# Kernel optimization log

Measured on AMD Instinct MI355X. Metric: run time of the kernel, lower is better.

## Reference

```python
import jax, jax.numpy as jnp
import numpy as np

N_NODES = 100000
N_EDGES = 1250000
IN_CH = 128
OUT_CH = 64


def setup_inputs() -> dict:
    key = jax.random.key(0)
    k1, k2, k3, k4 = jax.random.split(key, 4)
    x = jax.random.normal(k1, (N_NODES, IN_CH), dtype=jnp.float32)
    edge_index = jax.random.randint(k2, (2, N_EDGES), 0, N_NODES, dtype=jnp.int64)
    edge_weight = jax.random.uniform(k3, (N_EDGES,), dtype=jnp.float32)
    # Xavier-uniform weight, zero bias (as in reset_parameters)
    limit = float(np.sqrt(6.0 / (IN_CH + OUT_CH)))
    W = jax.random.uniform(k4, (IN_CH, OUT_CH), dtype=jnp.float32, minval=-limit, maxval=limit)
    b = jnp.zeros((OUT_CH,), dtype=jnp.float32)
    return {"x": x, "edge_index": edge_index, "edge_weight": edge_weight, "W": W, "b": b}


def reference(x, edge_index, edge_weight, W, b):
    # Dense transform: [N, in] @ [in, out] -> [N, out]
    h = jnp.matmul(x, W)
    row, col = edge_index[0], edge_index[1]
    n = h.shape[0]
    # Weighted in-degree via scatter-add on destination (row)
    deg = jnp.zeros((n,), dtype=h.dtype).at[row].add(edge_weight)
    # deg^-0.5 with inf (deg==0) replaced by 0
    deg_inv_sqrt = jnp.where(deg == 0, jnp.zeros_like(deg), deg ** -0.5)
    norm = deg_inv_sqrt[row] * deg_inv_sqrt[col]  # [E]
    # Gather source features, normalize, scatter-add to destinations
    out = jnp.zeros_like(h).at[row].add(h[col] * norm[:, None])
    return out + b
```

## Files before the change

kernel.cpp:

```cpp
#include <hip/hip_runtime.h>

#define N_NODES 100000
#define N_EDGES 1250000
#define IN_CH 128
#define OUT_CH 64

#define NPB 128
#define ACCS2 33
#define NBINS 782
#define HPAD 784
#define BINCAP_DEF 2048
#define NB1 256
#define B1T 512
#define CH1 ((N_EDGES + NB1 - 1) / NB1)
#define MAXU ((CH1 + B1T - 1) / B1T)
#define GEMM_BLOCKS ((N_NODES + 127) / 128)

#define QSCALE 8192.0f
#define QBIAS_F 8388608.0f
#define QBIAS_U 8388608u
#define INV_QSCALE 1.220703125e-4f
#define SCALE_DEG 33554432.0f
#define INV_SCALE_DEG 2.9802322387695312e-08f

typedef __attribute__((ext_vector_type(8))) short short8;
typedef __attribute__((ext_vector_type(4))) float f32x4;

__device__ inline unsigned int f2bf(float f) {
    unsigned int u = __float_as_uint(f);
    unsigned int r = ((u >> 16) & 1u) + 0x7FFFu;
    return (u + r) >> 16;
}
__device__ inline float bf_lo(unsigned int p) { return __uint_as_float(p << 16); }
__device__ inline float bf_hi(unsigned int p) { return __uint_as_float(p & 0xFFFF0000u); }

__device__ inline unsigned long long qpacks(unsigned int p, float sc) {
    unsigned int lo = (unsigned int)__float2int_rn(fmaf(bf_lo(p), sc, QBIAS_F));
    unsigned int hi = (unsigned int)__float2int_rn(fmaf(bf_hi(p), sc, QBIAS_F));
    return ((unsigned long long)hi << 32) | (unsigned long long)lo;
}

__global__ __launch_bounds__(256) void init_kernel(const float* __restrict__ W,
                                                   unsigned int* __restrict__ Wb) {
    int g = blockIdx.x * 256 + threadIdx.x;
    int c = g >> 8;
    int t4 = (g >> 6) & 3;
    int l = g & 63;
    int q = l >> 4, r15 = l & 15;
    unsigned int o[4];
#pragma unroll
    for (int jj = 0; jj < 4; ++jj) {
        float f0 = W[(c * 32 + q * 8 + 2 * jj)     * OUT_CH + t4 * 16 + r15];
        float f1 = W[(c * 32 + q * 8 + 2 * jj + 1) * OUT_CH + t4 * 16 + r15];
        o[jj] = f2bf(f0) | (f2bf(f1) << 16);
    }
    *(uint4*)(Wb + (size_t)g * 4) = make_uint4(o[0], o[1], o[2], o[3]);
}

__global__ __launch_bounds__(512) void fused_kernel(const float* __restrict__ x,
                                                    const unsigned int* __restrict__ Wb,
                                                    const int* __restrict__ ei,
                                                    int* __restrict__ hist2d,
                                                    unsigned int* __restrict__ hs) {
    __shared__ int hist[NBINS];
    const int tid = threadIdx.x;

    if (blockIdx.x < NB1) {
        for (int i = tid; i < NBINS; i += B1T) hist[i] = 0;
        __syncthreads();

        const int e0 = blockIdx.x * CH1;
        const int e1 = (e0 + CH1 < N_EDGES) ? e0 + CH1 : N_EDGES;
#pragma unroll
        for (int u = 0; u < MAXU; ++u) {
            int e = e0 + tid + u * B1T;
            if (e < e1) atomicAdd(&hist[ei[e] >> 7], 1);
        }
        __syncthreads();

        int* hrow = hist2d + blockIdx.x * HPAD;
        for (int i = tid; i < NBINS; i += B1T) hrow[i] = hist[i];
    } else {
        const int blk  = blockIdx.x - NB1;
        const int w    = tid >> 6;
        const int lane = tid & 63;
        const int q    = lane >> 4, r15 = lane & 15;
        const int node = blk * 128 + w * 16 + r15;
        const int nl   = (node < N_NODES) ? node : N_NODES - 1;
        const float* xrow = x + (size_t)nl * IN_CH;

        f32x4 acc[4];
#pragma unroll
        for (int t = 0; t < 4; ++t) acc[t] = (f32x4){0.f, 0.f, 0.f, 0.f};

#pragma unroll
        for (int c = 0; c < 4; ++c) {
            float4 xa = *(const float4*)(xrow + c * 32 + q * 8);
            float4 xb = *(const float4*)(xrow + c * 32 + q * 8 + 4);
            short8 bfrag;
            bfrag[0] = (short)f2bf(xa.x); bfrag[1] = (short)f2bf(xa.y);
            bfrag[2] = (short)f2bf(xa.z); bfrag[3] = (short)f2bf(xa.w);
            bfrag[4] = (short)f2bf(xb.x); bfrag[5] = (short)f2bf(xb.y);
            bfrag[6] = (short)f2bf(xb.z); bfrag[7] = (short)f2bf(xb.w);
#pragma unroll
            for (int t = 0; t < 4; ++t) {
                short8 afrag = *(const short8*)(Wb + (size_t)((c * 4 + t) * 64 + lane) * 4);
                acc[t] = __builtin_amdgcn_mfma_f32_16x16x32_bf16(afrag, bfrag, acc[t], 0, 0, 0);
            }
        }

        if (node < N_NODES) {
#pragma unroll
            for (int t = 0; t < 4; ++t) {
                unsigned int p0 = f2bf(acc[t][0]) | (f2bf(acc[t][1]) << 16);
                unsigned int p1 = f2bf(acc[t][2]) | (f2bf(acc[t][3]) << 16);
                *(uint2*)(hs + (size_t)node * 32 + t * 8 + q * 2) = make_uint2(p0, p1);
            }
        }
    }
}

__global__ __launch_bounds__(256) void scan_kernel(const int* __restrict__ hist2d,
                                                   int* __restrict__ offs2d,
                                                   int* __restrict__ mtot,
                                                   int bincap) {
    __shared__ int tmp[256];
    const int b = blockIdx.x, t = threadIdx.x;
    int v = hist2d[t * HPAD + b];
    int acc = v;
    tmp[t] = acc;
    __syncthreads();
#pragma unroll
    for (int d = 1; d < 256; d <<= 1) {
        int add = (t >= d) ? tmp[t - d] : 0;
        __syncthreads();
        acc += add;
        tmp[t] = acc;
        __syncthreads();
    }
    offs2d[b * 256 + t] = b * bincap + (acc - v);
    if (t == 255) mtot[b] = acc;
}

__global__ __launch_bounds__(B1T) void scatter_kernel(const int* __restrict__ ei,
                                                      const float* __restrict__ ew,
                                                      const int* __restrict__ offs2d,
                                                      int2* __restrict__ brec,
                                                      int bincap) {
    __shared__ int rank[NBINS];
    __shared__ int base[NBINS];
    const int t = threadIdx.x;
    for (int i = t; i < NBINS; i += B1T) {
        rank[i] = 0;
        base[i] = offs2d[i * 256 + blockIdx.x];
    }
    __syncthreads();

    const int e0 = blockIdx.x * CH1;
    const int e1 = (e0 + CH1 < N_EDGES) ? e0 + CH1 : N_EDGES;
#pragma unroll
    for (int u = 0; u < MAXU; ++u) {
        int e = e0 + t + u * B1T;
        if (e < e1) {
            int row = ei[e];
            int col = ei[N_EDGES + e];
            float w = ew[e];
            int bb = row >> 7;
            int rk = atomicAdd(&rank[bb], 1);
            int idx = base[bb] + rk;
            if (idx < (bb + 1) * bincap)
                brec[idx] = make_int2(((row & 127) << 17) | col, __float_as_int(w));
        }
    }
}

__global__ __launch_bounds__(256) void bin2_kernel(const int* __restrict__ mtot,
                                                   const int2* __restrict__ brec,
                                                   float* __restrict__ dis_g,
                                                   int bincap) {
    __shared__ int deg[NPB];
    const int t = threadIdx.x;
    const int b = blockIdx.x;
    if (t < NPB) deg[t] = 0;
    __syncthreads();

    const int rbase = b * bincap;
    int m = mtot[b];
    if (m > bincap) m = bincap;

    for (int j = t; j < m; j += 256) {
        int2 rec = brec[rbase + j];
        atomicAdd(&deg[rec.x >> 17], __float2int_rn(__int_as_float(rec.y) * SCALE_DEG));
    }
    __syncthreads();

    int node = b * NPB + t;
    if (t < NPB && node < N_NODES) {
        float d = (float)deg[t] * INV_SCALE_DEG;
        dis_g[node] = (d == 0.0f) ? 0.0f : (1.0f / sqrtf(d));
    }
}

__global__ __launch_bounds__(512) void gather_kernel(const int* __restrict__ mtot,
                                                     const int2* __restrict__ brec,
                                                     const uint4* __restrict__ hs,
                                                     const float* __restrict__ dis,
                                                     const float* __restrict__ b,
                                                     float* __restrict__ out,
                                                     int bincap) {
    __shared__ unsigned long long acc[NPB * ACCS2];
    __shared__ int cnt[NPB];
    const int tid = threadIdx.x;
    const int blk = blockIdx.x;
    for (int k = tid; k < NPB * ACCS2; k += 512) acc[k] = 0ull;
    if (tid < NPB) cnt[tid] = 0;
    __syncthreads();

    const int rbase = blk * bincap;
    int m = mtot[blk];
    if (m > bincap) m = bincap;

    const int wid = tid >> 6, lane = tid & 63;
    const int sub = lane >> 3, l8 = lane & 7;

    for (int j0 = wid * 32; j0 < m; j0 += 256) {
        bool ok[4];
        int rec[4];
        uint4 p[4];
        float sc[4];
#pragma unroll
        for (int s = 0; s < 4; ++s) {
            int jj = j0 + 8 * s + sub;
            ok[s] = jj < m;
            rec[s] = ok[s] ? brec[rbase + jj].x : 0;
        }
#pragma unroll
        for (int s = 0; s < 4; ++s) {
            p[s] = ok[s] ? hs[(size_t)(rec[s] & 0x1FFFF) * 8 + l8]
                         : make_uint4(0, 0, 0, 0);
            sc[s] = ok[s] ? QSCALE * dis[rec[s] & 0x1FFFF] : 0.0f;
        }
#pragma unroll
        for (int s = 0; s < 4; ++s) {
            if (ok[s]) {
                int ba = (rec[s] >> 17) * ACCS2 + 4 * l8;
                atomicAdd(&acc[ba + 0], qpacks(p[s].x, sc[s]));
                atomicAdd(&acc[ba + 1], qpacks(p[s].y, sc[s]));
                atomicAdd(&acc[ba + 2], qpacks(p[s].z, sc[s]));
                atomicAdd(&acc[ba + 3], qpacks(p[s].w, sc[s]));
                if (l8 == 0) atomicAdd(&cnt[rec[s] >> 17], 1);
            }
        }
    }
    __syncthreads();

    const unsigned int* acc32 = (const unsigned int*)acc;
    float bc = b[lane];
    int half = lane & 1, slot = lane >> 1;
#pragma unroll 4
    for (int r = 0; r < 16; ++r) {
        int nl = wid * 16 + r;
        int node = blk * NPB + nl;
        if (node < N_NODES) {
            unsigned int raw = acc32[(nl * ACCS2 + slot) * 2 + half];
            int qsum = (int)(raw - (unsigned int)cnt[nl] * QBIAS_U);
            float di = dis[node] * INV_QSCALE;
            out[(size_t)node * OUT_CH + lane] = (float)qsum * di + bc;
        }
    }
}

extern "C" void kernel_launch(void* const* d_in, const int* in_sizes, int n_in,
                              void* d_out, int out_size, void* d_ws, size_t ws_size,
                              hipStream_t stream) {
    const float* x  = (const float*)d_in[0];
    const int*   ei = (const int*)d_in[1];
    const float* ew = (const float*)d_in[2];
    const float* W  = (const float*)d_in[3];
    const float* b  = (const float*)d_in[4];
    float* out = (float*)d_out;

    unsigned int* hs = (unsigned int*)d_ws;
    unsigned int* Wb = hs + (size_t)N_NODES * 32;
    int* hist2d = (int*)(Wb + 4096);
    int* offs2d = hist2d + NB1 * HPAD;
    int* mtot   = offs2d + NBINS * 256;
    float* dis  = (float*)(mtot + 800);
    int2* brec  = (int2*)(dis + N_NODES);
    size_t used = (size_t)N_NODES * 32 + 4096 + (size_t)NB1 * HPAD
                + (size_t)NBINS * 256 + 800 + (size_t)N_NODES;
    size_t rem  = (ws_size / 4 > used) ? ws_size / 4 - used : 0;
    int bincap  = (int)(rem / (2 * (size_t)NBINS));
    if (bincap > BINCAP_DEF) bincap = BINCAP_DEF;

    init_kernel<<<4, 256, 0, stream>>>(W, Wb);
    fused_kernel<<<NB1 + GEMM_BLOCKS, 512, 0, stream>>>(x, Wb, ei, hist2d, hs);
    scan_kernel<<<NBINS, 256, 0, stream>>>(hist2d, offs2d, mtot, bincap);
    scatter_kernel<<<NB1, B1T, 0, stream>>>(ei, ew, offs2d, brec, bincap);
    bin2_kernel<<<NBINS, 256, 0, stream>>>(mtot, brec, dis, bincap);
    gather_kernel<<<NBINS, 512, 0, stream>>>(mtot, brec, (const uint4*)hs,
                                             dis, b, out, bincap);
}
```

Measured before the change: 171.9 us.

## Sort edges locally per block in shared memory, drop scan and scatter kernels

The edge-binning block of the fused kernel now builds its histogram, scans it in shared memory and writes its edge records already grouped by destination bin, along with a per-block scan table. Bin-degree and gather kernels then read each bin's records from 256 per-chunk segments using that table, instead of from a globally scattered bin array. This removes the global scan and scatter kernels, two launches, and the random global scatter writes. In exchange the fused kernel reserves about 40 KB of static shared memory, which the GEMM blocks also pay for and which may lower their occupancy. The gather kernel also gains a 256-wide shared scan and a serial per-thread segment copy.

Result: slower. 178.0 us (+3.6%).

```diff
diff --git a/kernel.cpp b/kernel.cpp
--- a/kernel.cpp
+++ b/kernel.cpp
@@ -8,8 +8,8 @@
 #define NPB 128
 #define ACCS2 33
 #define NBINS 782
-#define HPAD 784
-#define BINCAP_DEF 2048
+#define LSTRIDE 783
+#define RECCAP 2048
 #define NB1 256
 #define B1T 512
 #define CH1 ((N_EDGES + NB1 - 1) / NB1)
@@ -60,26 +60,81 @@
 __global__ __launch_bounds__(512) void fused_kernel(const float* __restrict__ x,
                                                     const unsigned int* __restrict__ Wb,
                                                     const int* __restrict__ ei,
-                                                    int* __restrict__ hist2d,
+                                                    const float* __restrict__ ew,
+                                                    int* __restrict__ lscan2d,
+                                                    int2* __restrict__ brec,
                                                     unsigned int* __restrict__ hs) {
-    __shared__ int hist[NBINS];
+    __shared__ int2 srec[CH1];
+    __shared__ int shist[NBINS];
+    __shared__ int sscan[NBINS + 2];
+    __shared__ int ssum[256];
     const int tid = threadIdx.x;
 
     if (blockIdx.x < NB1) {
-        for (int i = tid; i < NBINS; i += B1T) hist[i] = 0;
+        for (int i = tid; i < NBINS; i += B1T) shist[i] = 0;
         __syncthreads();
 
         const int e0 = blockIdx.x * CH1;
-        const int e1 = (e0 + CH1 < N_EDGES) ? e0 + CH1 : N_EDGES;
+        const int total = (e0 + CH1 < N_EDGES) ? CH1 : N_EDGES - e0;
+
+        int rowv[MAXU], colv[MAXU];
+        float wv[MAXU];
 #pragma unroll
         for (int u = 0; u < MAXU; ++u) {
             int e = e0 + tid + u * B1T;
-            if (e < e1) atomicAdd(&hist[ei[e] >> 7], 1);
-        }
-        __syncthreads();
-
-        int* hrow = hist2d + blockIdx.x * HPAD;
-        for (int i = tid; i < NBINS; i += B1T) hrow[i] = hist[i];
+            bool ok = (tid + u * B1T) < total;
+            rowv[u] = ok ? ei[e] : -1;
+            colv[u] = ok ? ei[N_EDGES + e] : 0;
+            wv[u]   = ok ? ew[e] : 0.0f;
+            if (ok) atomicAdd(&shist[rowv[u] >> 7], 1);
+        }
+        __syncthreads();
+
+        int a0 = 0, a1 = 0, a2 = 0, a3 = 0, part = 0;
+        const int b0 = tid * 4;
+        if (tid < 256) {
+            a0 = (b0 + 0 < NBINS) ? shist[b0 + 0] : 0;
+            a1 = (b0 + 1 < NBINS) ? shist[b0 + 1] : 0;
+            a2 = (b0 + 2 < NBINS) ? shist[b0 + 2] : 0;
+            a3 = (b0 + 3 < NBINS) ? shist[b0 + 3] : 0;
+            part = a0 + a1 + a2 + a3;
+            ssum[tid] = part;
+        }
+        __syncthreads();
+#pragma unroll
+        for (int d = 1; d < 256; d <<= 1) {
+            int add = 0;
+            if (tid >= d && tid < 256) add = ssum[tid - d];
+            __syncthreads();
+            if (tid < 256) ssum[tid] += add;
+            __syncthreads();
+        }
+        if (tid < 256) {
+            int base = ssum[tid] - part;
+            if (b0 + 0 <= NBINS) sscan[b0 + 0] = base;
+            if (b0 + 1 <= NBINS) sscan[b0 + 1] = base + a0;
+            if (b0 + 2 <= NBINS) sscan[b0 + 2] = base + a0 + a1;
+            if (b0 + 3 <= NBINS) sscan[b0 + 3] = base + a0 + a1 + a2;
+        }
+        __syncthreads();
+
+        for (int i = tid; i < NBINS; i += B1T) shist[i] = 0;
+        __syncthreads();
+
+#pragma unroll
+        for (int u = 0; u < MAXU; ++u) {
+            if (rowv[u] >= 0) {
+                int bb = rowv[u] >> 7;
+                int rk = atomicAdd(&shist[bb], 1);
+                srec[sscan[bb] + rk] = make_int2(((rowv[u] & 127) << 17) | colv[u],
+                                                 __float_as_int(wv[u]));
+            }
+        }
+        __syncthreads();
+
+        for (int i = tid; i < total; i += B1T) brec[e0 + i] = srec[i];
+        int* lrow = lscan2d + blockIdx.x * LSTRIDE;
+        for (int i = tid; i <= NBINS; i += B1T) lrow[i] = sscan[i];
     } else {
         const int blk  = blockIdx.x - NB1;
         const int w    = tid >> 6;
@@ -120,76 +175,20 @@
     }
 }
 
-__global__ __launch_bounds__(256) void scan_kernel(const int* __restrict__ hist2d,
-                                                   int* __restrict__ offs2d,
-                                                   int* __restrict__ mtot,
-                                                   int bincap) {
-    __shared__ int tmp[256];
-    const int b = blockIdx.x, t = threadIdx.x;
-    int v = hist2d[t * HPAD + b];
-    int acc = v;
-    tmp[t] = acc;
-    __syncthreads();
-#pragma unroll
-    for (int d = 1; d < 256; d <<= 1) {
-        int add = (t >= d) ? tmp[t - d] : 0;
-        __syncthreads();
-        acc += add;
-        tmp[t] = acc;
-        __syncthreads();
-    }
-    offs2d[b * 256 + t] = b * bincap + (acc - v);
-    if (t == 255) mtot[b] = acc;
-}
-
-__global__ __launch_bounds__(B1T) void scatter_kernel(const int* __restrict__ ei,
-                                                      const float* __restrict__ ew,
-                                                      const int* __restrict__ offs2d,
-                                                      int2* __restrict__ brec,
-                                                      int bincap) {
-    __shared__ int rank[NBINS];
-    __shared__ int base[NBINS];
-    const int t = threadIdx.x;
-    for (int i = t; i < NBINS; i += B1T) {
-        rank[i] = 0;
-        base[i] = offs2d[i * 256 + blockIdx.x];
-    }
-    __syncthreads();
-
-    const int e0 = blockIdx.x * CH1;
-    const int e1 = (e0 + CH1 < N_EDGES) ? e0 + CH1 : N_EDGES;
-#pragma unroll
-    for (int u = 0; u < MAXU; ++u) {
-        int e = e0 + t + u * B1T;
-        if (e < e1) {
-            int row = ei[e];
-            int col = ei[N_EDGES + e];
-            float w = ew[e];
-            int bb = row >> 7;
-            int rk = atomicAdd(&rank[bb], 1);
-            int idx = base[bb] + rk;
-            if (idx < (bb + 1) * bincap)
-                brec[idx] = make_int2(((row & 127) << 17) | col, __float_as_int(w));
-        }
-    }
-}
-
-__global__ __launch_bounds__(256) void bin2_kernel(const int* __restrict__ mtot,
+__global__ __launch_bounds__(256) void bin2_kernel(const int* __restrict__ lscan2d,
                                                    const int2* __restrict__ brec,
-                                                   float* __restrict__ dis_g,
-                                                   int bincap) {
+                                                   float* __restrict__ dis_g) {
     __shared__ int deg[NPB];
     const int t = threadIdx.x;
     const int b = blockIdx.x;
     if (t < NPB) deg[t] = 0;
     __syncthreads();
 
-    const int rbase = b * bincap;
-    int m = mtot[b];
-    if (m > bincap) m = bincap;
-
-    for (int j = t; j < m; j += 256) {
-        int2 rec = brec[rbase + j];
+    int st = lscan2d[t * LSTRIDE + b];
+    int en = lscan2d[t * LSTRIDE + b + 1];
+    const int2* seg = brec + (size_t)t * CH1;
+    for (int j = st; j < en; ++j) {
+        int2 rec = seg[j];
         atomicAdd(&deg[rec.x >> 17], __float2int_rn(__int_as_float(rec.y) * SCALE_DEG));
     }
     __syncthreads();
@@ -201,24 +200,51 @@
     }
 }
 
-__global__ __launch_bounds__(512) void gather_kernel(const int* __restrict__ mtot,
+__global__ __launch_bounds__(512) void gather_kernel(const int* __restrict__ lscan2d,
                                                      const int2* __restrict__ brec,
                                                      const uint4* __restrict__ hs,
                                                      const float* __restrict__ dis,
                                                      const float* __restrict__ b,
-                                                     float* __restrict__ out,
-                                                     int bincap) {
+                                                     float* __restrict__ out) {
     __shared__ unsigned long long acc[NPB * ACCS2];
     __shared__ int cnt[NPB];
+    __shared__ int recs[RECCAP];
+    __shared__ int segoff[256];
+    __shared__ int mtot_s;
     const int tid = threadIdx.x;
     const int blk = blockIdx.x;
     for (int k = tid; k < NPB * ACCS2; k += 512) acc[k] = 0ull;
     if (tid < NPB) cnt[tid] = 0;
-    __syncthreads();
-
-    const int rbase = blk * bincap;
-    int m = mtot[blk];
-    if (m > bincap) m = bincap;
+
+    int st = 0, len = 0;
+    if (tid < 256) {
+        st  = lscan2d[tid * LSTRIDE + blk];
+        len = lscan2d[tid * LSTRIDE + blk + 1] - st;
+        segoff[tid] = len;
+    }
+    __syncthreads();
+#pragma unroll
+    for (int d = 1; d < 256; d <<= 1) {
+        int add = 0;
+        if (tid >= d && tid < 256) add = segoff[tid - d];
+        __syncthreads();
+        if (tid < 256) segoff[tid] += add;
+        __syncthreads();
+    }
+    if (tid == 255) mtot_s = segoff[255];
+    __syncthreads();
+    int m = mtot_s;
+    if (m > RECCAP) m = RECCAP;
+
+    if (tid < 256) {
+        int off = segoff[tid] - len;
+        const int2* seg = brec + (size_t)tid * CH1 + st;
+        for (int i = 0; i < len; ++i) {
+            int p = off + i;
+            if (p < RECCAP) recs[p] = seg[i].x;
+        }
+    }
+    __syncthreads();
 
     const int wid = tid >> 6, lane = tid & 63;
     const int sub = lane >> 3, l8 = lane & 7;
@@ -232,7 +258,7 @@
         for (int s = 0; s < 4; ++s) {
             int jj = j0 + 8 * s + sub;
             ok[s] = jj < m;
-            rec[s] = ok[s] ? brec[rbase + jj].x : 0;
+            rec[s] = ok[s] ? recs[jj] : 0;
         }
 #pragma unroll
         for (int s = 0; s < 4; ++s) {
@@ -282,22 +308,15 @@
 
     unsigned int* hs = (unsigned int*)d_ws;
     unsigned int* Wb = hs + (size_t)N_NODES * 32;
-    int* hist2d = (int*)(Wb + 4096);
-    int* offs2d = hist2d + NB1 * HPAD;
-    int* mtot   = offs2d + NBINS * 256;
-    float* dis  = (float*)(mtot + 800);
-    int2* brec  = (int2*)(dis + N_NODES);
-    size_t used = (size_t)N_NODES * 32 + 4096 + (size_t)NB1 * HPAD
-                + (size_t)NBINS * 256 + 800 + (size_t)N_NODES;
-    size_t rem  = (ws_size / 4 > used) ? ws_size / 4 - used : 0;
-    int bincap  = (int)(rem / (2 * (size_t)NBINS));
-    if (bincap > BINCAP_DEF) bincap = BINCAP_DEF;
+    int* lscan2d = (int*)(Wb + 4096);
+    float* dis   = (float*)(lscan2d + NB1 * LSTRIDE);
+    int2* brec   = (int2*)(dis + N_NODES);
+    (void)ws_size; (void)in_sizes; (void)n_in; (void)out_size;
 
     init_kernel<<<4, 256, 0, stream>>>(W, Wb);
-    fused_kernel<<<NB1 + GEMM_BLOCKS, 512, 0, stream>>>(x, Wb, ei, hist2d, hs);
-    scan_kernel<<<NBINS, 256, 0, stream>>>(hist2d, offs2d, mtot, bincap);
-    scatter_kernel<<<NB1, B1T, 0, stream>>>(ei, ew, offs2d, brec, bincap);
-    bin2_kernel<<<NBINS, 256, 0, stream>>>(mtot, brec, dis, bincap);
-    gather_kernel<<<NBINS, 512, 0, stream>>>(mtot, brec, (const uint4*)hs,
-                                             dis, b, out, bincap);
-}
+    fused_kernel<<<NB1 + GEMM_BLOCKS, 512, 0, stream>>>(x, Wb, ei, ew,
+                                                        lscan2d, brec, hs);
+    bin2_kernel<<<NBINS, 256, 0, stream>>>(lscan2d, brec, dis);
+    gather_kernel<<<NBINS, 512, 0, stream>>>(lscan2d, brec, (const uint4*)hs,
+                                             dis, b, out);
+}
```
